# Performance work log

Measured on AMD Instinct MI355X. Metric: run time of the kernel, lower is better.

Reference implementation:

```python
import jax, jax.numpy as jnp
import numpy as np

EPS = 1e-3  # BatchNorm1d eps


def _fc_relu(x, W, b):
    return jax.nn.relu(x @ W + b)


def _fc_bn_relu(x, W, b, gamma, beta):
    # Linear -> BatchNorm1d (training mode: batch stats, biased var) -> ReLU
    h = x @ W + b
    m = jnp.mean(h, axis=0)
    v = jnp.var(h, axis=0)  # biased, matches torch BN normalization
    return jax.nn.relu((h - m) * jax.lax.rsqrt(v + EPS) * gamma + beta)


def _mmnet(img, tag, lat, lon, Wi, bi, gi, bti, Wt, bt, gt, btt, Wl, bl, gl, btl,
           W1, b1, W2, b2, W3, b3, W4, b4, W5, b5, W6, b6, W7, b7):
    img = _fc_bn_relu(img, Wi, bi, gi, bti)          # [B,300]
    tag = _fc_bn_relu(tag, Wt, bt, gt, btt)          # [B,300]
    loc = jnp.concatenate([lat, lon], axis=1)        # [B,2]
    loc = _fc_bn_relu(loc, Wl, bl, gl, btl)          # [B,10]
    x = jnp.concatenate([loc, img, tag], axis=1)     # [B,610]
    x = _fc_relu(x, W1, b1)                          # [B,2048]
    x = _fc_relu(x, W2, b2)                          # [B,2048]
    x = _fc_relu(x, W3, b3)                          # [B,1024]
    x = _fc_relu(x, W4, b4)                          # [B,1024]
    x = _fc_relu(x, W5, b5)                          # [B,512]
    x = _fc_relu(x, W6, b6)                          # [B,512]
    return x @ W7 + b7                               # [B,1]


def setup_inputs() -> dict:
    key = jax.random.key(0)
    ks = iter(jax.random.split(key, 64))
    B = 16384
    inp = {}
    inp['img_p'] = jax.random.normal(next(ks), (B, 300), jnp.float32)
    inp['tag_p'] = jax.random.normal(next(ks), (B, 300), jnp.float32)
    inp['lat_p'] = jax.random.uniform(next(ks), (B, 1), jnp.float32)
    inp['lon_p'] = jax.random.uniform(next(ks), (B, 1), jnp.float32)
    inp['img_n'] = jax.random.normal(next(ks), (B, 300), jnp.float32)
    inp['tag_n'] = jax.random.normal(next(ks), (B, 300), jnp.float32)
    inp['lat_n'] = jax.random.uniform(next(ks), (B, 1), jnp.float32)
    inp['lon_n'] = jax.random.uniform(next(ks), (B, 1), jnp.float32)
    inp['margin'] = 1

    def lin(din, dout):
        # matches l.weight.data.normal_(0, 0.01), bias zero; stored [din,dout]
        return (jax.random.normal(next(ks), (din, dout), jnp.float32) * 0.01,
                jnp.zeros((dout,), jnp.float32))

    inp['Wi'], inp['bi'] = lin(300, 300)
    inp['gi'], inp['bti'] = jnp.ones((300,), jnp.float32), jnp.zeros((300,), jnp.float32)
    inp['Wt'], inp['bt'] = lin(300, 300)
    inp['gt'], inp['btt'] = jnp.ones((300,), jnp.float32), jnp.zeros((300,), jnp.float32)
    inp['Wl'], inp['bl'] = lin(2, 10)
    inp['gl'], inp['btl'] = jnp.ones((10,), jnp.float32), jnp.zeros((10,), jnp.float32)
    inp['W1'], inp['b1'] = lin(610, 2048)
    inp['W2'], inp['b2'] = lin(2048, 2048)
    inp['W3'], inp['b3'] = lin(2048, 1024)
    inp['W4'], inp['b4'] = lin(1024, 1024)
    inp['W5'], inp['b5'] = lin(1024, 512)
    inp['W6'], inp['b6'] = lin(512, 512)
    inp['W7'], inp['b7'] = lin(512, 1)
    return inp


def reference(img_p, tag_p, lat_p, lon_p, img_n, tag_n, lat_n, lon_n,
              Wi, bi, gi, bti, Wt, bt, gt, btt, Wl, bl, gl, btl,
              W1, b1, W2, b2, W3, b3, W4, b4, W5, b5, W6, b6, W7, b7, margin):
    params = (Wi, bi, gi, bti, Wt, bt, gt, btt, Wl, bl, gl, btl,
              W1, b1, W2, b2, W3, b3, W4, b4, W5, b5, W6, b6, W7, b7)
    score_p = _mmnet(img_p, tag_p, lat_p, lon_p, *params)  # [B,1]
    score_n = _mmnet(img_n, tag_n, lat_n, lon_n, *params)  # [B,1]
    # vectorized replacement of the per-element python loop
    correct = jnp.sum((score_p - score_n)[:, 0] > margin).astype(jnp.int32)
    return score_p, score_n, correct
```

## Files before the change

kernel.cpp:

```cpp
#include <hip/hip_runtime.h>
#include <hip/hip_fp16.h>

typedef _Float16 half8 __attribute__((ext_vector_type(8)));
typedef float f32x16 __attribute__((ext_vector_type(16)));
typedef float f32x4 __attribute__((ext_vector_type(4)));

#define B_ROWS 16384
#define M_ALL  32768

__device__ __forceinline__ void glds16(void* lds, const void* g) {
  __builtin_amdgcn_global_load_lds(
      (const __attribute__((address_space(1))) unsigned int*)g,
      (__attribute__((address_space(3))) unsigned int*)lds, 16, 0, 0);
}

template<int EPI>
__global__ __launch_bounds__(256, 2)
void gemm128(const _Float16* __restrict__ A, const _Float16* __restrict__ Bt,
             const float* __restrict__ bias, _Float16* __restrict__ Cout,
             int M, int N, int K) {
  __shared__ _Float16 As[128 * 64];
  __shared__ _Float16 Bs[128 * 64];
  const int tid = threadIdx.x;
  const int w = tid >> 6, l = tid & 63;
  const int bm = blockIdx.y << 7, bn = blockIdx.x << 7;
  const int wm = (w >> 1) << 6, wn = (w & 1) << 6;
  const int l31 = l & 31, g5 = l >> 5, l7 = l & 7, l3 = l >> 3;

  f32x16 acc[2][2];
#pragma unroll
  for (int i = 0; i < 2; ++i)
#pragma unroll
    for (int j = 0; j < 2; ++j)
#pragma unroll
      for (int r = 0; r < 16; ++r) acc[i][j][r] = 0.f;

  const int schunk = (l7 ^ l3) * 8;
  const int srow = w * 32 + l3;

  for (int kt = 0; kt < K; kt += 64) {
#pragma unroll
    for (int c = 0; c < 4; ++c)
      glds16(&As[w * 2048 + c * 512],
             A + (size_t)(bm + srow + c * 8) * K + kt + schunk);
#pragma unroll
    for (int c = 0; c < 4; ++c)
      glds16(&Bs[w * 2048 + c * 512],
             Bt + (size_t)(bn + srow + c * 8) * K + kt + schunk);
    __syncthreads();
#pragma unroll
    for (int ks = 0; ks < 4; ++ks) {
      const int p0 = (((ks * 2 + g5) ^ l7)) * 8;
      half8 af[2], bf[2];
#pragma unroll
      for (int i = 0; i < 2; ++i)
        af[i] = *(const half8*)&As[(wm + i * 32 + l31) * 64 + p0];
#pragma unroll
      for (int i = 0; i < 2; ++i)
        bf[i] = *(const half8*)&Bs[(wn + i * 32 + l31) * 64 + p0];
#pragma unroll
      for (int i = 0; i < 2; ++i)
#pragma unroll
        for (int j = 0; j < 2; ++j)
          acc[i][j] = __builtin_amdgcn_mfma_f32_32x32x16_f16(af[i], bf[j], acc[i][j], 0, 0, 0);
    }
    __syncthreads();
  }

#pragma unroll
  for (int i = 0; i < 2; ++i)
#pragma unroll
    for (int j = 0; j < 2; ++j) {
      const int col = bn + wn + j * 32 + l31;
      float bv = 0.f;
      if (EPI == 1) bv = bias[col];
#pragma unroll
      for (int r = 0; r < 16; ++r) {
        const int row = bm + wm + i * 32 + (r & 3) + 8 * (r >> 2) + 4 * g5;
        const float v = acc[i][j][r] + bv;
        Cout[(size_t)row * N + col] = (_Float16)(EPI == 1 ? fmaxf(v, 0.f) : v);
      }
    }
}

#define BAR  __builtin_amdgcn_s_barrier()
#define LGKM0 asm volatile("s_waitcnt lgkmcnt(0)" ::: "memory")
#define LGKM8 asm volatile("s_waitcnt lgkmcnt(8)" ::: "memory")
#define VM4  asm volatile("s_waitcnt vmcnt(4)" ::: "memory")
#define VM0  asm volatile("s_waitcnt vmcnt(0)" ::: "memory")
#define LDA(AS, MH) \
  _Pragma("unroll") for (int mi_ = 0; mi_ < 4; ++mi_) { \
    _Pragma("unroll") for (int t2_ = 0; t2_ < 2; ++t2_) \
      a[mi_][t2_] = *(const half8*)((AS) + (wm * 128 + ((MH) * 4 + mi_) * 16 + l15) * 64 \
                                       + ((t2_ * 4 + kg) ^ l7) * 8); }
#define LDB(BS, NH, BR) \
  _Pragma("unroll") for (int nj_ = 0; nj_ < 2; ++nj_) { \
    _Pragma("unroll") for (int t2_ = 0; t2_ < 2; ++t2_) \
      BR[nj_][t2_] = *(const half8*)((BS) + (wn * 64 + ((NH) * 2 + nj_) * 16 + l15) * 64 \
                                        + ((t2_ * 4 + kg) ^ l7) * 8); }
#define MFMA16(MH, NH, BR) do { \
  __builtin_amdgcn_s_setprio(1); \
  _Pragma("unroll") for (int t2_ = 0; t2_ < 2; ++t2_) \
    _Pragma("unroll") for (int mi_ = 0; mi_ < 4; ++mi_) \
      _Pragma("unroll") for (int nj_ = 0; nj_ < 2; ++nj_) \
        acc[(MH) * 4 + mi_][(NH) * 2 + nj_] = __builtin_amdgcn_mfma_f32_16x16x32_f16( \
            a[mi_][t2_], BR[nj_][t2_], acc[(MH) * 4 + mi_][(NH) * 2 + nj_], 0, 0, 0); \
  __builtin_amdgcn_s_setprio(0); } while (0)

__global__ __launch_bounds__(512, 2)
void gemm256(const _Float16* __restrict__ A, const _Float16* __restrict__ Bt,
             const float* __restrict__ bias, _Float16* __restrict__ Cout,
             int M, int N, int K) {
  __shared__ _Float16 smem[4 * 256 * 64];
  const int tid = threadIdx.x;
  const int w = tid >> 6, l = tid & 63;
  const int nwg = gridDim.x * gridDim.y;
  const int orig = blockIdx.y * gridDim.x + blockIdx.x;
  const int wgid = (orig & 7) * (nwg >> 3) + (orig >> 3);
  const int bx = wgid % gridDim.x, by = wgid / gridDim.x;
  const int bm = by << 8, bn = bx << 8;
  const int wm = w >> 2, wn = w & 3;
  const int l15 = l & 15, kg = l >> 4, l7 = l & 7;

  f32x4 acc[8][4];
#pragma unroll
  for (int i = 0; i < 8; ++i)
#pragma unroll
    for (int j = 0; j < 4; ++j)
#pragma unroll
      for (int r = 0; r < 4; ++r) acc[i][j][r] = 0.f;

  const int srow = tid >> 3;
  const int schunk = ((tid & 7) ^ (srow & 7)) * 8;
  const _Float16* aBase = A + (size_t)(bm + srow) * K + schunk;
  const _Float16* bBase = Bt + (size_t)(bn + srow) * K + schunk;
  const int NT = K >> 6, NI = NT >> 1;

  auto stA = [&](int buf, int h, int t) {
    const _Float16* s = aBase + (size_t)(h * 128) * K + (size_t)t * 64;
    _Float16* d = smem + buf * 16384 + h * 8192 + w * 512;
    glds16(d, s);
    glds16(d + 4096, s + (size_t)64 * K);
  };
  auto stB = [&](int buf, int h, int t) {
    const _Float16* s = bBase + (size_t)(h * 128) * K + (size_t)t * 64;
    _Float16* d = smem + 32768 + buf * 16384 + h * 8192 + w * 512;
    glds16(d, s);
    glds16(d + 4096, s + (size_t)64 * K);
  };

  stB(0, 0, 0); stA(0, 0, 0); stA(0, 1, 0); stB(0, 1, 0);
  stB(1, 0, 1); stA(1, 0, 1);
  VM4; BAR;

  const _Float16* as0 = smem;
  const _Float16* as1 = smem + 16384;
  const _Float16* bs0 = smem + 32768;
  const _Float16* bs1 = smem + 49152;

  half8 a[4][2], b0r[2][2], b1r[2][2];

  for (int i = 0; i < NI; ++i) {
    const int t1 = 2 * i + 1, tn0 = 2 * i + 2, tn1 = 2 * i + 3;
    const bool s0 = tn0 < NT, s1 = tn1 < NT;
    LDA(as0, 0); LDB(bs0, 0, b0r);
    stA(1, 1, t1);
    LGKM8; BAR; LGKM0; MFMA16(0, 0, b0r); BAR;
    LDB(bs0, 1, b1r);
    stB(1, 1, t1);
    BAR; LGKM0; MFMA16(0, 1, b1r); BAR;
    LDA(as0, 1);
    if (s0) stB(0, 0, tn0);
    BAR; LGKM0; MFMA16(1, 1, b1r); BAR;
    if (s0) stA(0, 0, tn0);
    BAR; LGKM0; MFMA16(1, 0, b0r);
    if (s0) { VM4; } else { VM0; }
    BAR;
    LDA(as1, 0); LDB(bs1, 0, b0r);
    if (s0) stA(0, 1, tn0);
    LGKM8; BAR; LGKM0; MFMA16(0, 0, b0r); BAR;
    LDB(bs1, 1, b1r);
    if (s0) stB(0, 1, tn0);
    BAR; LGKM0; MFMA16(0, 1, b1r); BAR;
    LDA(as1, 1);
    if (s1) stB(1, 0, tn1);
    BAR; LGKM0; MFMA16(1, 1, b1r); BAR;
    if (s1) stA(1, 0, tn1);
    BAR; LGKM0; MFMA16(1, 0, b0r);
    if (s1) { VM4; }
    BAR;
  }

#pragma unroll
  for (int nj = 0; nj < 4; ++nj) {
    const int col = bn + wn * 64 + nj * 16 + l15;
    const float bv = bias[col];
#pragma unroll
    for (int mi = 0; mi < 8; ++mi) {
#pragma unroll
      for (int r = 0; r < 4; ++r) {
        const int row = bm + wm * 128 + mi * 16 + (kg << 2) + r;
        Cout[(size_t)row * N + col] = (_Float16)fmaxf(acc[mi][nj][r] + bv, 0.f);
      }
    }
  }
}

__global__ void tpose_pad(const float* __restrict__ src, _Float16* __restrict__ dst,
                          int Ks, int Ns, int Kd, int Nd) {
  __shared__ float t[32][33];
  const int k0 = blockIdx.x * 32, n0 = blockIdx.y * 32;
  const int tx = threadIdx.x & 31, ty = threadIdx.x >> 5;
#pragma unroll
  for (int i = ty; i < 32; i += 8) {
    const int k = k0 + i, n = n0 + tx;
    t[i][tx] = (k < Ks && n < Ns) ? src[(size_t)k * Ns + n] : 0.f;
  }
  __syncthreads();
#pragma unroll
  for (int i = ty; i < 32; i += 8)
    dst[(size_t)(n0 + i) * Kd + (k0 + tx)] = (_Float16)t[tx][i];
}

__global__ void cvt_in_k(const float* __restrict__ xp, const float* __restrict__ xn,
                         _Float16* __restrict__ X, int C, int Cp) {
  const size_t total = (size_t)M_ALL * Cp;
  const size_t stride = (size_t)gridDim.x * blockDim.x;
  for (size_t idx = (size_t)blockIdx.x * blockDim.x + threadIdx.x; idx < total; idx += stride) {
    const int r = (int)(idx / Cp);
    const int c = (int)(idx - (size_t)r * Cp);
    float v = 0.f;
    if (c < C) v = (r < B_ROWS) ? xp[(size_t)r * C + c] : xn[(size_t)(r - B_ROWS) * C + c];
    X[idx] = (_Float16)v;
  }
}

__global__ void stats_k(const _Float16* __restrict__ h, float* __restrict__ sums, int ldh, int C) {
  const int half = blockIdx.y;
  const int nr = B_ROWS / gridDim.x;
  const int r0 = half * B_ROWS + blockIdx.x * nr;
  for (int c = threadIdx.x; c < C; c += blockDim.x) {
    float s = 0.f, q = 0.f;
    for (int r = 0; r < nr; ++r) {
      const float v = (float)h[(size_t)(r0 + r) * ldh + c];
      s += v; q += v * v;
    }
    atomicAdd(&sums[(half * 2 + 0) * 384 + c], s);
    atomicAdd(&sums[(half * 2 + 1) * 384 + c], q);
  }
}

__global__ void bn_apply_k(const _Float16* __restrict__ h, const float* __restrict__ sums,
                           const float* __restrict__ gamma, const float* __restrict__ beta,
                           _Float16* __restrict__ X1, int coff) {
  const size_t total = (size_t)M_ALL * 300;
  const size_t stride = (size_t)gridDim.x * blockDim.x;
  for (size_t idx = (size_t)blockIdx.x * blockDim.x + threadIdx.x; idx < total; idx += stride) {
    const int r = (int)(idx / 300);
    const int c = (int)(idx - (size_t)r * 300);
    const int hf = r >> 14;
    const float mean = sums[(hf * 2 + 0) * 384 + c] * (1.f / 16384.f);
    const float ms   = sums[(hf * 2 + 1) * 384 + c] * (1.f / 16384.f);
    const float inv = rsqrtf(ms - mean * mean + 1e-3f) * gamma[c];
    const float y = ((float)h[(size_t)r * 384 + c] - mean) * inv + beta[c];
    X1[(size_t)r * 640 + coff + c] = (_Float16)fmaxf(y, 0.f);
  }
}

__global__ void loc_k(const float* __restrict__ lat_p, const float* __restrict__ lon_p,
                      const float* __restrict__ lat_n, const float* __restrict__ lon_n,
                      const float* __restrict__ Wl, const float* __restrict__ gl,
                      const float* __restrict__ btl, _Float16* __restrict__ X1) {
  const int j = blockIdx.x, half = blockIdx.y;
  const float* lat = half ? lat_n : lat_p;
  const float* lon = half ? lon_n : lon_p;
  const float w0 = Wl[j], w1 = Wl[10 + j];
  const int t = threadIdx.x;
  float s = 0.f, q = 0.f;
  for (int r = t; r < B_ROWS; r += 256) {
    const float v = lat[r] * w0 + lon[r] * w1;
    s += v; q += v * v;
  }
  __shared__ float rs[256], rq[256];
  rs[t] = s; rq[t] = q;
  __syncthreads();
  for (int o = 128; o; o >>= 1) {
    if (t < o) { rs[t] += rs[t + o]; rq[t] += rq[t + o]; }
    __syncthreads();
  }
  const float mean = rs[0] * (1.f / 16384.f);
  const float var = rq[0] * (1.f / 16384.f) - mean * mean;
  const float inv = rsqrtf(var + 1e-3f) * gl[j];
  const float bb = btl[j];
  for (int r = t; r < B_ROWS; r += 256) {
    const float v = lat[r] * w0 + lon[r] * w1;
    const float y = (v - mean) * inv + bb;
    X1[(size_t)(half * B_ROWS + r) * 640 + j] = (_Float16)fmaxf(y, 0.f);
  }
}

__global__ void scores_k(const _Float16* __restrict__ Y, const float* __restrict__ w7,
                         const float* __restrict__ b7, float* __restrict__ out) {
  const int row = blockIdx.x * 4 + (threadIdx.x >> 6);
  const int l = threadIdx.x & 63;
  const half8 v = *(const half8*)(Y + (size_t)row * 512 + l * 8);
  float s = 0.f;
#pragma unroll
  for (int j = 0; j < 8; ++j) s += (float)v[j] * w7[l * 8 + j];
#pragma unroll
  for (int o = 32; o; o >>= 1) s += __shfl_down(s, o);
  if (l == 0) out[row] = s + b7[0];
}

__global__ void correct_k(const float* __restrict__ sc, const int* __restrict__ mg,
                          float* __restrict__ dst) {
  __shared__ int red[256];
  const int t = threadIdx.x;
  const float m = (float)(*mg);
  int c = 0;
  for (int i = t; i < B_ROWS; i += 256)
    c += (sc[i] - sc[B_ROWS + i]) > m ? 1 : 0;
  red[t] = c;
  __syncthreads();
  for (int o = 128; o; o >>= 1) {
    if (t < o) red[t] += red[t + o];
    __syncthreads();
  }
  if (t == 0) dst[0] = (float)red[0];
}

extern "C" void kernel_launch(void* const* d_in, const int* in_sizes, int n_in,
                              void* d_out, int out_size, void* d_ws, size_t ws_size,
                              hipStream_t stream) {
  const float* img_p = (const float*)d_in[0];
  const float* tag_p = (const float*)d_in[1];
  const float* lat_p = (const float*)d_in[2];
  const float* lon_p = (const float*)d_in[3];
  const float* img_n = (const float*)d_in[4];
  const float* tag_n = (const float*)d_in[5];
  const float* lat_n = (const float*)d_in[6];
  const float* lon_n = (const float*)d_in[7];
  const int*   margin = (const int*)d_in[8];
  const float* Wi = (const float*)d_in[9];
  const float* gi = (const float*)d_in[11];
  const float* bti = (const float*)d_in[12];
  const float* Wt = (const float*)d_in[13];
  const float* gt = (const float*)d_in[15];
  const float* btt = (const float*)d_in[16];
  const float* Wl = (const float*)d_in[17];
  const float* gl = (const float*)d_in[19];
  const float* btl = (const float*)d_in[20];
  const float* W1 = (const float*)d_in[21]; const float* b1 = (const float*)d_in[22];
  const float* W2 = (const float*)d_in[23]; const float* b2 = (const float*)d_in[24];
  const float* W3 = (const float*)d_in[25]; const float* b3 = (const float*)d_in[26];
  const float* W4 = (const float*)d_in[27]; const float* b4 = (const float*)d_in[28];
  const float* W5 = (const float*)d_in[29]; const float* b5 = (const float*)d_in[30];
  const float* W6 = (const float*)d_in[31]; const float* b6 = (const float*)d_in[32];
  const float* W7 = (const float*)d_in[33]; const float* b7 = (const float*)d_in[34];
  float* out = (float*)d_out;

  char* ws = (char*)d_ws;
  size_t off = 0;
  auto alloc = [&](size_t bytes) -> void* {
    void* p = ws + off;
    off += (bytes + 255) & ~(size_t)255;
    return p;
  };
  _Float16* WiT = (_Float16*)alloc((size_t)384 * 320 * 2);
  _Float16* WtT = (_Float16*)alloc((size_t)384 * 320 * 2);
  _Float16* W1T = (_Float16*)alloc((size_t)2048 * 640 * 2);
  _Float16* W2T = (_Float16*)alloc((size_t)2048 * 2048 * 2);
  _Float16* W3T = (_Float16*)alloc((size_t)1024 * 2048 * 2);
  _Float16* W4T = (_Float16*)alloc((size_t)1024 * 1024 * 2);
  _Float16* W5T = (_Float16*)alloc((size_t)512 * 1024 * 2);
  _Float16* W6T = (_Float16*)alloc((size_t)512 * 512 * 2);
  float* sbuf = (float*)alloc((size_t)2 * 4 * 384 * 4);
  _Float16* X1 = (_Float16*)alloc((size_t)M_ALL * 640 * 2);

  const size_t persist = off;
  const size_t avail = ws_size > persist ? ws_size - persist : 0;
  int CR = 4096;
  if (avail >= (size_t)2 * 32768 * 2048 * 2) CR = 32768;
  else if (avail >= (size_t)2 * 16384 * 2048 * 2) CR = 16384;
  else if (avail >= (size_t)2 * 8192 * 2048 * 2) CR = 8192;
  _Float16* Ya = (_Float16*)(ws + persist);
  _Float16* Yb = Ya + (size_t)CR * 2048;
  _Float16* Ximg = Ya;
  _Float16* hbuf = (_Float16*)((char*)Ya + (size_t)M_ALL * 320 * 2);

  (void)hipMemsetAsync(X1, 0, (size_t)M_ALL * 640 * 2, stream);
  (void)hipMemsetAsync(sbuf, 0, (size_t)2 * 4 * 384 * 4, stream);

  tpose_pad<<<dim3(10, 12), 256, 0, stream>>>(Wi, WiT, 300, 300, 320, 384);
  tpose_pad<<<dim3(10, 12), 256, 0, stream>>>(Wt, WtT, 300, 300, 320, 384);
  tpose_pad<<<dim3(20, 64), 256, 0, stream>>>(W1, W1T, 610, 2048, 640, 2048);
  tpose_pad<<<dim3(64, 64), 256, 0, stream>>>(W2, W2T, 2048, 2048, 2048, 2048);
  tpose_pad<<<dim3(64, 32), 256, 0, stream>>>(W3, W3T, 2048, 1024, 2048, 1024);
  tpose_pad<<<dim3(32, 32), 256, 0, stream>>>(W4, W4T, 1024, 1024, 1024, 1024);
  tpose_pad<<<dim3(32, 16), 256, 0, stream>>>(W5, W5T, 1024, 512, 1024, 512);
  tpose_pad<<<dim3(16, 16), 256, 0, stream>>>(W6, W6T, 512, 512, 512, 512);

  cvt_in_k<<<2048, 256, 0, stream>>>(img_p, img_n, Ximg, 300, 320);
  gemm128<2><<<dim3(3, 256), 256, 0, stream>>>(Ximg, WiT, nullptr, hbuf, M_ALL, 384, 320);
  stats_k<<<dim3(128, 2), 256, 0, stream>>>(hbuf, sbuf, 384, 300);
  bn_apply_k<<<2048, 256, 0, stream>>>(hbuf, sbuf, gi, bti, X1, 10);
  cvt_in_k<<<2048, 256, 0, stream>>>(tag_p, tag_n, Ximg, 300, 320);
  gemm128<2><<<dim3(3, 256), 256, 0, stream>>>(Ximg, WtT, nullptr, hbuf, M_ALL, 384, 320);
  stats_k<<<dim3(128, 2), 256, 0, stream>>>(hbuf, sbuf + 4 * 384, 384, 300);
  bn_apply_k<<<2048, 256, 0, stream>>>(hbuf, sbuf + 4 * 384, gt, btt, X1, 310);
  loc_k<<<dim3(10, 2), 256, 0, stream>>>(lat_p, lon_p, lat_n, lon_n, Wl, gl, btl, X1);

  for (int c0 = 0; c0 < M_ALL; c0 += CR) {
    const int rb = CR / 128, rb2 = CR / 256;
    const _Float16* Xc = X1 + (size_t)c0 * 640;
    gemm256<<<dim3(8, rb2), 512, 0, stream>>>(Xc, W1T, b1, Ya, CR, 2048, 640);
    gemm256<<<dim3(8, rb2), 512, 0, stream>>>(Ya, W2T, b2, Yb, CR, 2048, 2048);
    gemm256<<<dim3(4, rb2), 512, 0, stream>>>(Yb, W3T, b3, Ya, CR, 1024, 2048);
    gemm256<<<dim3(4, rb2), 512, 0, stream>>>(Ya, W4T, b4, Yb, CR, 1024, 1024);
    gemm128<1><<<dim3(4, rb), 256, 0, stream>>>(Yb, W5T, b5, Ya, CR, 512, 1024);
    gemm128<1><<<dim3(4, rb), 256, 0, stream>>>(Ya, W6T, b6, Yb, CR, 512, 512);
    scores_k<<<CR / 4, 256, 0, stream>>>(Yb, W7, b7, out + c0);
  }

  correct_k<<<1, 256, 0, stream>>>(out, margin, out + 32768);
}
```

Baseline: 951.4 us.

## Double-buffer LDS fragment registers and cut barriers in 256-tile GEMM main loop

Restructures the gemm256 inner loop to keep separate even/odd A and B register fragments, so LDS reads for the next quadrant are issued ahead of the MFMAs that consume the current ones. Most per-quadrant barriers and explicit lgkmcnt waits are removed, leaving compiler-inserted waits and fewer workgroup barriers per half-tile. Launch bounds drop to one block per CU to give room for the extra fragment registers. This trades occupancy for fewer synchronisation stalls and risks LDS read/write hazards if the remaining barriers do not cover the async global-to-LDS stores.

```diff
diff --git a/kernel.cpp b/kernel.cpp
--- a/kernel.cpp
+++ b/kernel.cpp
@@ -83,31 +83,30 @@
     }
 }
 
-#define BAR  __builtin_amdgcn_s_barrier()
-#define LGKM0 asm volatile("s_waitcnt lgkmcnt(0)" ::: "memory")
-#define LGKM8 asm volatile("s_waitcnt lgkmcnt(8)" ::: "memory")
 #define VM4  asm volatile("s_waitcnt vmcnt(4)" ::: "memory")
 #define VM0  asm volatile("s_waitcnt vmcnt(0)" ::: "memory")
-#define LDA(AS, MH) \
+#define BARRIER do { asm volatile("" ::: "memory"); __builtin_amdgcn_s_barrier(); \
+                     asm volatile("" ::: "memory"); } while (0)
+#define LDA(AS, MH, AR) \
   _Pragma("unroll") for (int mi_ = 0; mi_ < 4; ++mi_) { \
     _Pragma("unroll") for (int t2_ = 0; t2_ < 2; ++t2_) \
-      a[mi_][t2_] = *(const half8*)((AS) + (wm * 128 + ((MH) * 4 + mi_) * 16 + l15) * 64 \
-                                       + ((t2_ * 4 + kg) ^ l7) * 8); }
+      AR[mi_][t2_] = *(const half8*)((AS) + (wm * 128 + ((MH) * 4 + mi_) * 16 + l15) * 64 \
+                                        + ((t2_ * 4 + kg) ^ l7) * 8); }
 #define LDB(BS, NH, BR) \
   _Pragma("unroll") for (int nj_ = 0; nj_ < 2; ++nj_) { \
     _Pragma("unroll") for (int t2_ = 0; t2_ < 2; ++t2_) \
       BR[nj_][t2_] = *(const half8*)((BS) + (wn * 64 + ((NH) * 2 + nj_) * 16 + l15) * 64 \
                                         + ((t2_ * 4 + kg) ^ l7) * 8); }
-#define MFMA16(MH, NH, BR) do { \
+#define MFMAQ(MH, NH, AR, BR) do { \
   __builtin_amdgcn_s_setprio(1); \
   _Pragma("unroll") for (int t2_ = 0; t2_ < 2; ++t2_) \
     _Pragma("unroll") for (int mi_ = 0; mi_ < 4; ++mi_) \
       _Pragma("unroll") for (int nj_ = 0; nj_ < 2; ++nj_) \
         acc[(MH) * 4 + mi_][(NH) * 2 + nj_] = __builtin_amdgcn_mfma_f32_16x16x32_f16( \
-            a[mi_][t2_], BR[nj_][t2_], acc[(MH) * 4 + mi_][(NH) * 2 + nj_], 0, 0, 0); \
+            AR[mi_][t2_], BR[nj_][t2_], acc[(MH) * 4 + mi_][(NH) * 2 + nj_], 0, 0, 0); \
   __builtin_amdgcn_s_setprio(0); } while (0)
 
-__global__ __launch_bounds__(512, 2)
+__global__ __launch_bounds__(512, 1)
 void gemm256(const _Float16* __restrict__ A, const _Float16* __restrict__ Bt,
              const float* __restrict__ bias, _Float16* __restrict__ Cout,
              int M, int N, int K) {
@@ -151,44 +150,43 @@
 
   stB(0, 0, 0); stA(0, 0, 0); stA(0, 1, 0); stB(0, 1, 0);
   stB(1, 0, 1); stA(1, 0, 1);
-  VM4; BAR;
+  VM4; BARRIER;
 
   const _Float16* as0 = smem;
   const _Float16* as1 = smem + 16384;
   const _Float16* bs0 = smem + 32768;
   const _Float16* bs1 = smem + 49152;
 
-  half8 a[4][2], b0r[2][2], b1r[2][2];
+  half8 aE[4][2], aO[4][2], bE[2][2], bO[2][2];
+  LDA(as0, 0, aE); LDB(bs0, 0, bE);
 
   for (int i = 0; i < NI; ++i) {
     const int t1 = 2 * i + 1, tn0 = 2 * i + 2, tn1 = 2 * i + 3;
     const bool s0 = tn0 < NT, s1 = tn1 < NT;
-    LDA(as0, 0); LDB(bs0, 0, b0r);
-    stA(1, 1, t1);
-    LGKM8; BAR; LGKM0; MFMA16(0, 0, b0r); BAR;
-    LDB(bs0, 1, b1r);
-    stB(1, 1, t1);
-    BAR; LGKM0; MFMA16(0, 1, b1r); BAR;
-    LDA(as0, 1);
+    LDA(as0, 1, aO);  stA(1, 1, t1);
+    MFMAQ(0, 0, aE, bE);
+    LDB(bs0, 1, bO);  stB(1, 1, t1);
+    MFMAQ(1, 0, aO, bE);
+    BARRIER;
     if (s0) stB(0, 0, tn0);
-    BAR; LGKM0; MFMA16(1, 1, b1r); BAR;
+    MFMAQ(1, 1, aO, bO);
     if (s0) stA(0, 0, tn0);
-    BAR; LGKM0; MFMA16(1, 0, b0r);
+    MFMAQ(0, 1, aE, bO);
     if (s0) { VM4; } else { VM0; }
-    BAR;
-    LDA(as1, 0); LDB(bs1, 0, b0r);
-    if (s0) stA(0, 1, tn0);
-    LGKM8; BAR; LGKM0; MFMA16(0, 0, b0r); BAR;
-    LDB(bs1, 1, b1r);
-    if (s0) stB(0, 1, tn0);
-    BAR; LGKM0; MFMA16(0, 1, b1r); BAR;
-    LDA(as1, 1);
+    BARRIER;
+    LDA(as1, 0, aE); LDB(bs1, 0, bE);
+    LDA(as1, 1, aO);  if (s0) stA(0, 1, tn0);
+    MFMAQ(0, 0, aE, bE);
+    LDB(bs1, 1, bO);  if (s0) stB(0, 1, tn0);
+    MFMAQ(1, 0, aO, bE);
+    BARRIER;
     if (s1) stB(1, 0, tn1);
-    BAR; LGKM0; MFMA16(1, 1, b1r); BAR;
+    MFMAQ(1, 1, aO, bO);
     if (s1) stA(1, 0, tn1);
-    BAR; LGKM0; MFMA16(1, 0, b0r);
+    MFMAQ(0, 1, aE, bO);
     if (s1) { VM4; }
-    BAR;
+    BARRIER;
+    if (i + 1 < NI) { LDA(as0, 0, aE); LDB(bs0, 0, bE); }
   }
 
 #pragma unroll
```

After: 1.373 ms. +44.3%, slower.
